# Performance work log

Measured on AMD Instinct MI355X. Metric: run time of the kernel, lower is better.

The kernel has to match this reference:

```python
import jax, jax.numpy as jnp
import numpy as np

N_RES = 320
C_Z = 128
NUM_HEAD = 4
HEAD_DIM = C_Z // NUM_HEAD  # 32
LN_EPS = 1e-5


def layer_norm(x, scale, offset):
    mean = jnp.mean(x, axis=-1, keepdims=True)
    var = jnp.var(x, axis=-1, keepdims=True)
    return (x - mean) * jax.lax.rsqrt(var + LN_EPS) * scale + offset


def setup_inputs() -> dict:
    key = jax.random.key(0)
    ks = jax.random.split(key, 12)
    d = {
        'pair_act': jax.random.normal(ks[0], (N_RES, N_RES, C_Z), jnp.float32),
        'affine_act': jax.random.normal(ks[1], (N_RES, N_RES, C_Z), jnp.float32),
        'pair_mask': jnp.ones((N_RES, N_RES), jnp.float32),
        'pair_ln_scale': jnp.ones((C_Z,), jnp.float32),
        'pair_ln_offset': jnp.zeros((C_Z,), jnp.float32),
        'affine_ln_scale': jnp.ones((C_Z,), jnp.float32),
        'affine_ln_offset': jnp.zeros((C_Z,), jnp.float32),
        'feat_2d_weights': jax.random.normal(ks[2], (C_Z, NUM_HEAD), jnp.float32) / 0.8796256610342398,
        'query_w': jax.random.normal(ks[3], (C_Z, NUM_HEAD, HEAD_DIM), jnp.float32) * 0.05,
        'key_w': jax.random.normal(ks[4], (C_Z, NUM_HEAD, HEAD_DIM), jnp.float32) * 0.05,
        'value_w': jax.random.normal(ks[5], (C_Z, NUM_HEAD, HEAD_DIM), jnp.float32) * 0.05,
        'gating_w': jax.random.normal(ks[6], (C_Z, NUM_HEAD, HEAD_DIM), jnp.float32) * 0.05,
        'output_w': jax.random.normal(ks[7], (NUM_HEAD, HEAD_DIM, C_Z), jnp.float32) * 0.05,
    }
    return d


def reference(pair_act, affine_act, pair_mask,
              pair_ln_scale, pair_ln_offset, affine_ln_scale, affine_ln_offset,
              feat_2d_weights, query_w, key_w, value_w, gating_w, output_w):
    # orientation == 'per_row' -> no swapaxes
    pair_ln = layer_norm(pair_act, pair_ln_scale, pair_ln_offset)          # [N,N,c]
    affine_ln = layer_norm(affine_act, affine_ln_scale, affine_ln_offset)  # [N,N,c]

    # padding bias [N,1,1,N]
    bias = (1e9 * (pair_mask - 1.0))[:, None, None, :]
    # nonbatched pair bias [H,N,N]
    nonbatched_bias = jnp.einsum('qkc,ch->hqk', affine_ln, feat_2d_weights)

    # attention (q_data == m_data == pair_ln)
    scale = HEAD_DIM ** (-0.5)
    q = jnp.einsum('bqa,ahc->bqhc', pair_ln, query_w) * scale
    k = jnp.einsum('bka,ahc->bkhc', pair_ln, key_w)
    v = jnp.einsum('bka,ahc->bkhc', pair_ln, value_w)

    logits = jnp.einsum('bqhc,bkhc->bhqk', q, k) + bias + nonbatched_bias[None]
    weights = jax.nn.softmax(logits, axis=-1)
    weighted_avg = jnp.einsum('bhqk,bkhc->bqhc', weights, v)

    gate = jax.nn.sigmoid(jnp.einsum('bqc,chv->bqhv', pair_ln, gating_w))
    weighted_avg = weighted_avg * gate

    out = jnp.einsum('bqhc,hco->bqo', weighted_avg, output_w)  # [N,N,c_z]
    return out
```

## Files before the change

### kernel.cpp

```cpp
#include <hip/hip_runtime.h>
#include <hip/hip_bf16.h>

#define N_RES 320
#define C_Z   128
#define NH    4
#define HD    32
#define M_TOT (N_RES*N_RES)
#define LN_EPS 1e-5f
#define QSCALE 0.17677669529663687f

typedef __attribute__((ext_vector_type(8))) short short8;
typedef __attribute__((ext_vector_type(4))) float floatx4;

#define OFF_MASK 0
#define OFF_PLS  102400
#define OFF_PLO  102528
#define OFF_ALS  102656
#define OFF_ALO  102784
#define OFF_FWT  102912
#define OFF_WQT  104960
#define OFF_WKT  121344
#define OFF_WVT  137728
#define OFF_WGT  154112
#define OFF_WOT  170496
#define ARENA_N  186880

__device__ __forceinline__ float u16_to_f(unsigned short s){
    union { unsigned u; float f; } v; v.u = ((unsigned)s) << 16; return v.f;
}
__device__ __forceinline__ unsigned short bf16r(float f){
    union { __hip_bfloat16 b; unsigned short s; } v; v.b = __float2bfloat16(f); return v.s;
}
__device__ __forceinline__ unsigned pack2(float a, float b){
    return (unsigned)bf16r(a) | ((unsigned)bf16r(b) << 16);
}
__device__ __forceinline__ float ld_dual(const void* s, size_t i, bool isbf){
    return isbf ? u16_to_f(((const unsigned short*)s)[i]) : ((const float*)s)[i];
}

__global__ __launch_bounds__(256) void k_conv_all(
    const void* __restrict__ s_mask, const void* __restrict__ s_pls,
    const void* __restrict__ s_plo,  const void* __restrict__ s_als,
    const void* __restrict__ s_alo,  const void* __restrict__ s_fw,
    const void* __restrict__ s_wq,   const void* __restrict__ s_wk,
    const void* __restrict__ s_wv,   const void* __restrict__ s_wg,
    const void* __restrict__ s_wo,
    unsigned short* __restrict__ arena, const unsigned* __restrict__ probe)
{
    int gid = blockIdx.x * 256 + threadIdx.x;
    bool isbf = (probe[0] & 0xffffu) != 0;
    float val;
    if (gid < OFF_PLS)      val = ld_dual(s_mask, gid, isbf);
    else if (gid < OFF_PLO) val = ld_dual(s_pls, gid - OFF_PLS, isbf);
    else if (gid < OFF_ALS) val = ld_dual(s_plo, gid - OFF_PLO, isbf);
    else if (gid < OFF_ALO) val = ld_dual(s_als, gid - OFF_ALS, isbf);
    else if (gid < OFF_FWT) val = ld_dual(s_alo, gid - OFF_ALO, isbf);
    else if (gid < OFF_WQT){
        int local = gid - OFF_FWT, hh = local >> 7, c = local & 127;
        val = (hh < 4) ? ld_dual(s_fw, c*NH + hh, isbf) : 0.0f;
    } else if (gid < OFF_WOT){
        int seg = (gid - OFF_WQT) >> 14;
        int local = (gid - OFF_WQT) & 16383;
        int hc = local >> 7, z = local & 127;
        const void* src = (seg == 0) ? s_wq : (seg == 1) ? s_wk : (seg == 2) ? s_wv : s_wg;
        val = ld_dual(src, z*128 + hc, isbf);
    } else {
        int local = gid - OFF_WOT, o = local >> 7, hc = local & 127;
        val = ld_dual(s_wo, hc*128 + o, isbf);
    }
    arena[gid] = bf16r(val);
}

__global__ __launch_bounds__(256) void k_affine_ln_nb(
    const void* __restrict__ affine,
    const unsigned short* __restrict__ sc, const unsigned short* __restrict__ of,
    const unsigned short* __restrict__ fwpT, float* __restrict__ nb,
    const unsigned* __restrict__ probe)
{
    int tid = threadIdx.x, lane = tid & 63, wave = tid >> 6;
    int c16 = lane & 15, quad = lane >> 4, rb = quad * 4;
    int m0 = blockIdx.x * 64 + wave * 16;
    bool isbf = (probe[0] & 0xffffu) != 0;

    float x[32];
    if (isbf){
        const short8* a8 = (const short8*)affine;
        #pragma unroll
        for (int ks = 0; ks < 4; ++ks){
            short8 t = a8[(size_t)(m0 + c16)*16 + ks*4 + quad];
            #pragma unroll
            for (int j = 0; j < 8; ++j) x[ks*8+j] = u16_to_f((unsigned short)t[j]);
        }
    } else {
        const floatx4* a4 = (const floatx4*)affine;
        #pragma unroll
        for (int ks = 0; ks < 4; ++ks){
            floatx4 f0 = a4[(size_t)(m0 + c16)*32 + ks*8 + quad*2];
            floatx4 f1 = a4[(size_t)(m0 + c16)*32 + ks*8 + quad*2 + 1];
            #pragma unroll
            for (int j = 0; j < 4; ++j){ x[ks*8+j] = f0[j]; x[ks*8+4+j] = f1[j]; }
        }
    }
    float s = 0.f, ss = 0.f;
    #pragma unroll
    for (int j = 0; j < 32; ++j){ s += x[j]; ss += x[j]*x[j]; }
    s  += __shfl_xor(s, 16, 64);  s  += __shfl_xor(s, 32, 64);
    ss += __shfl_xor(ss, 16, 64); ss += __shfl_xor(ss, 32, 64);
    float mean = s * (1.0f/128.0f);
    float var  = ss * (1.0f/128.0f) - mean*mean;
    float rs   = rsqrtf(var + LN_EPS);

    const short8* sc8 = (const short8*)sc;
    const short8* of8 = (const short8*)of;
    short8 lf[4], lg[4];
    #pragma unroll
    for (int ks = 0; ks < 4; ++ks){
        short8 scv = sc8[ks*4 + quad], ofv = of8[ks*4 + quad];
        #pragma unroll
        for (int j = 0; j < 8; ++j){
            float l = (x[ks*8+j] - mean) * rs * u16_to_f((unsigned short)scv[j])
                    + u16_to_f((unsigned short)ofv[j]);
            unsigned short hi = bf16r(l);
            lf[ks][j] = (short)hi;
            lg[ks][j] = (short)bf16r(l - u16_to_f(hi));
        }
    }
    floatx4 acc = {0.f, 0.f, 0.f, 0.f};
    const short8* fw8 = (const short8*)fwpT;
    #pragma unroll
    for (int ks = 0; ks < 4; ++ks){
        short8 fwf = fw8[c16*16 + ks*4 + quad];
        acc = __builtin_amdgcn_mfma_f32_16x16x32_bf16(lf[ks], fwf, acc, 0, 0, 0);
        acc = __builtin_amdgcn_mfma_f32_16x16x32_bf16(lg[ks], fwf, acc, 0, 0, 0);
    }
    if (c16 < 4)
        *(floatx4*)&nb[(size_t)c16 * M_TOT + m0 + rb] = acc;
}

__global__ __launch_bounds__(256) void k_pair_ln(
    const void* __restrict__ pair,
    const unsigned short* __restrict__ sc, const unsigned short* __restrict__ of,
    unsigned short* __restrict__ pl, const unsigned* __restrict__ probe)
{
    int tid = threadIdx.x, lane = tid & 63, wave = tid >> 6;
    int c16 = lane & 15, quad = lane >> 4;
    int m0 = blockIdx.x * 64 + wave * 16;
    bool isbf = (probe[0] & 0xffffu) != 0;

    float x[32];
    if (isbf){
        const short8* a8 = (const short8*)pair;
        #pragma unroll
        for (int ks = 0; ks < 4; ++ks){
            short8 t = a8[(size_t)(m0 + c16)*16 + ks*4 + quad];
            #pragma unroll
            for (int j = 0; j < 8; ++j) x[ks*8+j] = u16_to_f((unsigned short)t[j]);
        }
    } else {
        const floatx4* a4 = (const floatx4*)pair;
        #pragma unroll
        for (int ks = 0; ks < 4; ++ks){
            floatx4 f0 = a4[(size_t)(m0 + c16)*32 + ks*8 + quad*2];
            floatx4 f1 = a4[(size_t)(m0 + c16)*32 + ks*8 + quad*2 + 1];
            #pragma unroll
            for (int j = 0; j < 4; ++j){ x[ks*8+j] = f0[j]; x[ks*8+4+j] = f1[j]; }
        }
    }
    float s = 0.f, ss = 0.f;
    #pragma unroll
    for (int j = 0; j < 32; ++j){ s += x[j]; ss += x[j]*x[j]; }
    s  += __shfl_xor(s, 16, 64);  s  += __shfl_xor(s, 32, 64);
    ss += __shfl_xor(ss, 16, 64); ss += __shfl_xor(ss, 32, 64);
    float mean = s * (1.0f/128.0f);
    float var  = ss * (1.0f/128.0f) - mean*mean;
    float rs   = rsqrtf(var + LN_EPS);

    const short8* sc8 = (const short8*)sc;
    const short8* of8 = (const short8*)of;
    short8* pl8 = (short8*)pl;
    #pragma unroll
    for (int ks = 0; ks < 4; ++ks){
        short8 scv = sc8[ks*4 + quad], ofv = of8[ks*4 + quad];
        short8 lf;
        #pragma unroll
        for (int j = 0; j < 8; ++j){
            float l = (x[ks*8+j] - mean) * rs * u16_to_f((unsigned short)scv[j])
                    + u16_to_f((unsigned short)ofv[j]);
            lf[j] = (short)bf16r(l);
        }
        pl8[(size_t)(m0 + c16)*16 + ks*4 + quad] = lf;
    }
}

__global__ __launch_bounds__(512, 4) void k_attn(
    const unsigned short* __restrict__ pl,
    const unsigned short* __restrict__ wqT, const unsigned short* __restrict__ wkT,
    const unsigned short* __restrict__ wvT, const unsigned short* __restrict__ wgT,
    const unsigned short* __restrict__ maskc, const float* __restrict__ nb,
    unsigned short* __restrict__ wab)
{
    __shared__ __align__(16) unsigned short Ks[320*40];
    __shared__ __align__(16) unsigned short Vt[32*328];
    __shared__ __align__(16) unsigned short Pbuf[8*640];
    __shared__ __align__(16) float biasl[320];

    int b = blockIdx.x, h = blockIdx.y;
    int tid = threadIdx.x, lane = tid & 63, wave = tid >> 6;
    int c16 = lane & 15, quad = lane >> 4, rb = quad * 4;

    const short8* plrow8 = (const short8*)(pl + (size_t)b * N_RES * C_Z);
    const short8* Ks8 = (const short8*)Ks;
    const short8* Vt8 = (const short8*)Vt;
    const short8* wqT8 = (const short8*)wqT;
    const short8* wgT8 = (const short8*)wgT;
    unsigned short* Pw = Pbuf + wave * 640;
    const short8* Pb8 = (const short8*)Pw;
    floatx4 Z = {0.f, 0.f, 0.f, 0.f};

    if (tid < 320)
        biasl[tid] = 1e9f * (u16_to_f(maskc[(size_t)b * N_RES + tid]) - 1.0f);

    #pragma unroll 1
    for (int t = wave; t < 80; t += 8){
        int isV = (t >= 40) ? 1 : 0;
        int r = isV ? t - 40 : t;
        int ct = (r >= 20) ? 1 : 0;
        int mt = (r >= 20) ? r - 20 : r;
        int hc = h*HD + ct*16 + c16;
        const short8* WT8 = (const short8*)(isV ? wvT : wkT);
        short8 bw[4], a[4];
        #pragma unroll
        for (int ks = 0; ks < 4; ++ks){
            bw[ks] = WT8[hc*16 + ks*4 + quad];
            a[ks]  = plrow8[(mt*16 + c16)*16 + ks*4 + quad];
        }
        floatx4 acc = Z;
        if (!isV){
            #pragma unroll
            for (int ks = 0; ks < 4; ++ks)
                acc = __builtin_amdgcn_mfma_f32_16x16x32_bf16(a[ks], bw[ks], acc, 0, 0, 0);
            #pragma unroll
            for (int i = 0; i < 4; ++i)
                Ks[(mt*16 + rb + i)*40 + ct*16 + c16] = bf16r(acc[i]);
        } else {
            #pragma unroll
            for (int ks = 0; ks < 4; ++ks)
                acc = __builtin_amdgcn_mfma_f32_16x16x32_bf16(bw[ks], a[ks], acc, 0, 0, 0);
            #pragma unroll
            for (int i = 0; i < 4; ++i)
                Vt[(ct*16 + rb + i)*328 + mt*16 + c16] = bf16r(acc[i]);
        }
    }
    __syncthreads();

    #pragma unroll 1
    for (int mt = wave; mt < 20; mt += 8){
        int m0 = mt * 16;
        short8 plf[4];
        #pragma unroll
        for (int ks = 0; ks < 4; ++ks)
            plf[ks] = plrow8[(m0 + c16)*16 + ks*4 + quad];

        floatx4 q0 = Z, q1 = Z;
        #pragma unroll
        for (int ks = 0; ks < 4; ++ks){
            short8 w0 = wqT8[(h*HD + c16)*16 + ks*4 + quad];
            short8 w1 = wqT8[(h*HD + 16 + c16)*16 + ks*4 + quad];
            q0 = __builtin_amdgcn_mfma_f32_16x16x32_bf16(w0, plf[ks], q0, 0, 0, 0);
            q1 = __builtin_amdgcn_mfma_f32_16x16x32_bf16(w1, plf[ks], q1, 0, 0, 0);
        }
        {
            uint2 pk0 = { pack2(q0[0]*QSCALE, q0[1]*QSCALE), pack2(q0[2]*QSCALE, q0[3]*QSCALE) };
            uint2 pk1 = { pack2(q1[0]*QSCALE, q1[1]*QSCALE), pack2(q1[2]*QSCALE, q1[3]*QSCALE) };
            *(uint2*)&Pw[c16*40 + quad*4]      = pk0;
            *(uint2*)&Pw[c16*40 + 16 + quad*4] = pk1;
        }
        short8 qf = Pb8[c16*5 + quad];

        float mrow = -3.0e38f, lrow = 0.f;
        floatx4 acc0 = Z, acc1 = Z;
        const float* nbq = nb + (size_t)h * M_TOT + (size_t)(m0 + c16) * N_RES;

        #pragma unroll 1
        for (int kt2 = 0; kt2 < 10; ++kt2){
            int k0 = kt2 * 32;
            short8 kfa = Ks8[(k0 + c16)*5 + quad];
            short8 kfb = Ks8[(k0 + 16 + c16)*5 + quad];
            floatx4 sa = __builtin_amdgcn_mfma_f32_16x16x32_bf16(kfa, qf, Z, 0, 0, 0);
            floatx4 sb = __builtin_amdgcn_mfma_f32_16x16x32_bf16(kfb, qf, Z, 0, 0, 0);
            floatx4 nba = *(const floatx4*)&nbq[k0 + quad*4];
            floatx4 nbb = *(const floatx4*)&nbq[k0 + 16 + quad*4];
            floatx4 bia = *(const floatx4*)&biasl[k0 + quad*4];
            floatx4 bib = *(const floatx4*)&biasl[k0 + 16 + quad*4];
            float tm = -3.0e38f;
            #pragma unroll
            for (int i = 0; i < 4; ++i){
                sa[i] += nba[i] + bia[i];
                sb[i] += nbb[i] + bib[i];
                tm = fmaxf(tm, fmaxf(sa[i], sb[i]));
            }
            tm = fmaxf(tm, __shfl_xor(tm, 16, 64));
            tm = fmaxf(tm, __shfl_xor(tm, 32, 64));
            float mn = fmaxf(mrow, tm);
            float alpha = __expf(mrow - mn);
            mrow = mn;
            float pa[4], pb[4], tsum = 0.f;
            #pragma unroll
            for (int i = 0; i < 4; ++i){
                pa[i] = __expf(sa[i] - mn);
                pb[i] = __expf(sb[i] - mn);
                tsum += pa[i] + pb[i];
            }
            tsum += __shfl_xor(tsum, 16, 64);
            tsum += __shfl_xor(tsum, 32, 64);
            lrow = lrow * alpha + tsum;
            uint2 wa = { pack2(pa[0], pa[1]), pack2(pa[2], pa[3]) };
            uint2 wb = { pack2(pb[0], pb[1]), pack2(pb[2], pb[3]) };
            *(uint2*)&Pw[c16*40 + quad*4]      = wa;
            *(uint2*)&Pw[c16*40 + 16 + quad*4] = wb;
            short8 pf = Pb8[c16*5 + quad];
            short8 v0 = Vt8[c16*41 + kt2*4 + quad];
            short8 v1 = Vt8[(16 + c16)*41 + kt2*4 + quad];
            #pragma unroll
            for (int i = 0; i < 4; ++i){
                float al = __shfl(alpha, rb + i, 64);
                acc0[i] *= al; acc1[i] *= al;
            }
            acc0 = __builtin_amdgcn_mfma_f32_16x16x32_bf16(pf, v0, acc0, 0, 0, 0);
            acc1 = __builtin_amdgcn_mfma_f32_16x16x32_bf16(pf, v1, acc1, 0, 0, 0);
        }

        floatx4 g0 = Z, g1 = Z;
        #pragma unroll
        for (int ks = 0; ks < 4; ++ks){
            short8 w0 = wgT8[(h*HD + c16)*16 + ks*4 + quad];
            short8 w1 = wgT8[(h*HD + 16 + c16)*16 + ks*4 + quad];
            g0 = __builtin_amdgcn_mfma_f32_16x16x32_bf16(plf[ks], w0, g0, 0, 0, 0);
            g1 = __builtin_amdgcn_mfma_f32_16x16x32_bf16(plf[ks], w1, g1, 0, 0, 0);
        }
        #pragma unroll
        for (int i = 0; i < 4; ++i){
            float li = __shfl(lrow, rb + i, 64);
            float inv = 1.0f / li;
            float o0 = acc0[i] * inv * (1.0f/(1.0f + __expf(-g0[i])));
            float o1 = acc1[i] * inv * (1.0f/(1.0f + __expf(-g1[i])));
            size_t orow = (size_t)h * (M_TOT*HD) + (size_t)(b*N_RES + m0 + rb + i) * HD;
            wab[orow + c16]      = bf16r(o0);
            wab[orow + 16 + c16] = bf16r(o1);
        }
    }
}

__global__ __launch_bounds__(256, 4) void k_outproj(
    const unsigned short* __restrict__ wab, const unsigned short* __restrict__ woT,
    void* __restrict__ out, const unsigned* __restrict__ probe)
{
    int tid = threadIdx.x, lane = tid & 63, wave = tid >> 6;
    int c16 = lane & 15, quad = lane >> 4, rb = quad * 4;
    int m0 = blockIdx.x * 64 + wave * 16;
    bool isbf = (probe[0] & 0xffffu) != 0;

    const short8* wab8 = (const short8*)wab;
    const short8* woT8 = (const short8*)woT;
    floatx4 Z = {0.f, 0.f, 0.f, 0.f};

    short8 a[4];
    #pragma unroll
    for (int ks = 0; ks < 4; ++ks)
        a[ks] = wab8[(size_t)ks * (M_TOT*4) + (size_t)(m0 + c16)*4 + quad];

    #pragma unroll 1
    for (int nt = 0; nt < 8; ++nt){
        floatx4 acc = Z;
        #pragma unroll
        for (int ks = 0; ks < 4; ++ks){
            short8 bf = woT8[(nt*16 + c16)*16 + ks*4 + quad];
            acc = __builtin_amdgcn_mfma_f32_16x16x32_bf16(a[ks], bf, acc, 0, 0, 0);
        }
        #pragma unroll
        for (int i = 0; i < 4; ++i){
            size_t idx = (size_t)(m0 + rb + i)*C_Z + nt*16 + c16;
            if (isbf) ((unsigned short*)out)[idx] = bf16r(acc[i]);
            else      ((float*)out)[idx] = acc[i];
        }
    }
}

extern "C" void kernel_launch(void* const* d_in, const int* in_sizes, int n_in,
                              void* d_out, int out_size, void* d_ws, size_t ws_size,
                              hipStream_t stream)
{
    const unsigned* probe = (const unsigned*)d_in[3];

    char* w = (char*)d_ws;
    unsigned short* arena = (unsigned short*)w;
    unsigned short* mask_c = arena + OFF_MASK;
    unsigned short* pls_c  = arena + OFF_PLS;
    unsigned short* plo_c  = arena + OFF_PLO;
    unsigned short* als_c  = arena + OFF_ALS;
    unsigned short* alo_c  = arena + OFF_ALO;
    unsigned short* fwT_c  = arena + OFF_FWT;
    unsigned short* wqT_c  = arena + OFF_WQT;
    unsigned short* wkT_c  = arena + OFF_WKT;
    unsigned short* wvT_c  = arena + OFF_WVT;
    unsigned short* wgT_c  = arena + OFF_WGT;
    unsigned short* woT_c  = arena + OFF_WOT;
    float*          nb     = (float*)(w + 524288);
    unsigned short* pl     = (unsigned short*)(w + 2162688);
    unsigned short* wab    = (unsigned short*)(w + 28377088);

    k_conv_all<<<730, 256, 0, stream>>>(d_in[2], d_in[3], d_in[4], d_in[5], d_in[6],
                                        d_in[7], d_in[8], d_in[9], d_in[10], d_in[11],
                                        d_in[12], arena, probe);
    k_affine_ln_nb<<<1600, 256, 0, stream>>>(d_in[1], als_c, alo_c, fwT_c, nb, probe);
    k_pair_ln    <<<1600, 256, 0, stream>>>(d_in[0], pls_c, plo_c, pl, probe);
    k_attn       <<<dim3(N_RES, NH), 512, 0, stream>>>(pl, wqT_c, wkT_c, wvT_c, wgT_c,
                                                       mask_c, nb, wab);
    k_outproj    <<<1600, 256, 0, stream>>>(wab, woT_c, d_out, probe);
}
```

Before: 416.8 us.

## Replace LDS P/Q staging with cross-lane permlane transposes, fold log2e into exp2

Result: slower. 444.2 us (+6.6%).

```diff
diff --git a/kernel.cpp b/kernel.cpp
--- a/kernel.cpp
+++ b/kernel.cpp
@@ -8,9 +8,11 @@
 #define M_TOT (N_RES*N_RES)
 #define LN_EPS 1e-5f
 #define QSCALE 0.17677669529663687f
+#define LOG2E  1.4426950408889634f
 
 typedef __attribute__((ext_vector_type(8))) short short8;
 typedef __attribute__((ext_vector_type(4))) float floatx4;
+typedef __attribute__((ext_vector_type(4))) unsigned uintx4;
 
 #define OFF_MASK 0
 #define OFF_PLS  102400
@@ -36,6 +38,32 @@
 }
 __device__ __forceinline__ float ld_dual(const void* s, size_t i, bool isbf){
     return isbf ? u16_to_f(((const unsigned short*)s)[i]) : ((const float*)s)[i];
+}
+
+__device__ __forceinline__ short8 xpose_frag(unsigned A0, unsigned A1,
+                                             unsigned B0, unsigned B1, int lane)
+{
+#if __has_builtin(__builtin_amdgcn_permlane32_swap) && __has_builtin(__builtin_amdgcn_permlane16_swap)
+    (void)lane;
+    auto uv0 = __builtin_amdgcn_permlane32_swap(A0, B0, false, false);
+    auto uv1 = __builtin_amdgcn_permlane32_swap(A1, B1, false, false);
+    auto t02 = __builtin_amdgcn_permlane16_swap(uv0[0], uv0[1], false, false);
+    auto t13 = __builtin_amdgcn_permlane16_swap(uv1[0], uv1[1], false, false);
+    uintx4 u = { t02[0], t13[0], t02[1], t13[1] };
+#else
+    bool hi32 = lane >= 32, oddq = (lane & 16) != 0;
+    unsigned A0x = __shfl_xor(A0, 32, 64), B0x = __shfl_xor(B0, 32, 64);
+    unsigned A1x = __shfl_xor(A1, 32, 64), B1x = __shfl_xor(B1, 32, 64);
+    unsigned U0 = hi32 ? B0x : A0, V0 = hi32 ? B0 : A0x;
+    unsigned U1 = hi32 ? B1x : A1, V1 = hi32 ? B1 : A1x;
+    unsigned U0x = __shfl_xor(U0, 16, 64), V0x = __shfl_xor(V0, 16, 64);
+    unsigned U1x = __shfl_xor(U1, 16, 64), V1x = __shfl_xor(V1, 16, 64);
+    unsigned T0 = oddq ? V0x : U0, T2 = oddq ? V0 : U0x;
+    unsigned T1 = oddq ? V1x : U1, T3 = oddq ? V1 : U1x;
+    uintx4 u = { T0, T1, T2, T3 };
+#endif
+    union { uintx4 u; short8 s; } cvt; cvt.u = u;
+    return cvt.s;
 }
 
 __global__ __launch_bounds__(256) void k_conv_all(
@@ -133,6 +161,7 @@
         acc = __builtin_amdgcn_mfma_f32_16x16x32_bf16(lf[ks], fwf, acc, 0, 0, 0);
         acc = __builtin_amdgcn_mfma_f32_16x16x32_bf16(lg[ks], fwf, acc, 0, 0, 0);
     }
+    acc = acc * LOG2E;
     if (c16 < 4)
         *(floatx4*)&nb[(size_t)c16 * M_TOT + m0 + rb] = acc;
 }
@@ -192,7 +221,7 @@
     }
 }
 
-__global__ __launch_bounds__(512, 4) void k_attn(
+__global__ __launch_bounds__(512, 6) void k_attn(
     const unsigned short* __restrict__ pl,
     const unsigned short* __restrict__ wqT, const unsigned short* __restrict__ wkT,
     const unsigned short* __restrict__ wvT, const unsigned short* __restrict__ wgT,
@@ -201,7 +230,6 @@
 {
     __shared__ __align__(16) unsigned short Ks[320*40];
     __shared__ __align__(16) unsigned short Vt[32*328];
-    __shared__ __align__(16) unsigned short Pbuf[8*640];
     __shared__ __align__(16) float biasl[320];
 
     int b = blockIdx.x, h = blockIdx.y;
@@ -213,12 +241,10 @@
     const short8* Vt8 = (const short8*)Vt;
     const short8* wqT8 = (const short8*)wqT;
     const short8* wgT8 = (const short8*)wgT;
-    unsigned short* Pw = Pbuf + wave * 640;
-    const short8* Pb8 = (const short8*)Pw;
     floatx4 Z = {0.f, 0.f, 0.f, 0.f};
 
     if (tid < 320)
-        biasl[tid] = 1e9f * (u16_to_f(maskc[(size_t)b * N_RES + tid]) - 1.0f);
+        biasl[tid] = (LOG2E * 1e9f) * (u16_to_f(maskc[(size_t)b * N_RES + tid]) - 1.0f);
 
     #pragma unroll 1
     for (int t = wave; t < 80; t += 8){
@@ -261,23 +287,23 @@
         for (int ks = 0; ks < 4; ++ks)
             plf[ks] = plrow8[(m0 + c16)*16 + ks*4 + quad];
 
-        floatx4 q0 = Z, q1 = Z;
+        floatx4 q0 = Z, q1 = Z, g0v = Z, g1v = Z;
         #pragma unroll
         for (int ks = 0; ks < 4; ++ks){
             short8 w0 = wqT8[(h*HD + c16)*16 + ks*4 + quad];
             short8 w1 = wqT8[(h*HD + 16 + c16)*16 + ks*4 + quad];
             q0 = __builtin_amdgcn_mfma_f32_16x16x32_bf16(w0, plf[ks], q0, 0, 0, 0);
             q1 = __builtin_amdgcn_mfma_f32_16x16x32_bf16(w1, plf[ks], q1, 0, 0, 0);
-        }
-        {
-            uint2 pk0 = { pack2(q0[0]*QSCALE, q0[1]*QSCALE), pack2(q0[2]*QSCALE, q0[3]*QSCALE) };
-            uint2 pk1 = { pack2(q1[0]*QSCALE, q1[1]*QSCALE), pack2(q1[2]*QSCALE, q1[3]*QSCALE) };
-            *(uint2*)&Pw[c16*40 + quad*4]      = pk0;
-            *(uint2*)&Pw[c16*40 + 16 + quad*4] = pk1;
-        }
-        short8 qf = Pb8[c16*5 + quad];
-
-        float mrow = -3.0e38f, lrow = 0.f;
+            short8 u0 = wgT8[(h*HD + c16)*16 + ks*4 + quad];
+            short8 u1 = wgT8[(h*HD + 16 + c16)*16 + ks*4 + quad];
+            g0v = __builtin_amdgcn_mfma_f32_16x16x32_bf16(u0, plf[ks], g0v, 0, 0, 0);
+            g1v = __builtin_amdgcn_mfma_f32_16x16x32_bf16(u1, plf[ks], g1v, 0, 0, 0);
+        }
+        const float QS = QSCALE * LOG2E;
+        short8 qf = xpose_frag(pack2(q0[0]*QS, q0[1]*QS), pack2(q0[2]*QS, q0[3]*QS),
+                               pack2(q1[0]*QS, q1[1]*QS), pack2(q1[2]*QS, q1[3]*QS), lane);
+
+        float mrow = -3.0e38f, lpart = 0.f;
         floatx4 acc0 = Z, acc1 = Z;
         const float* nbq = nb + (size_t)h * M_TOT + (size_t)(m0 + c16) * N_RES;
 
@@ -288,66 +314,54 @@
             short8 kfb = Ks8[(k0 + 16 + c16)*5 + quad];
             floatx4 sa = __builtin_amdgcn_mfma_f32_16x16x32_bf16(kfa, qf, Z, 0, 0, 0);
             floatx4 sb = __builtin_amdgcn_mfma_f32_16x16x32_bf16(kfb, qf, Z, 0, 0, 0);
-            floatx4 nba = *(const floatx4*)&nbq[k0 + quad*4];
-            floatx4 nbb = *(const floatx4*)&nbq[k0 + 16 + quad*4];
-            floatx4 bia = *(const floatx4*)&biasl[k0 + quad*4];
-            floatx4 bib = *(const floatx4*)&biasl[k0 + 16 + quad*4];
-            float tm = -3.0e38f;
+            floatx4 nba = *(const floatx4*)&nbq[k0 + rb];
+            floatx4 nbb = *(const floatx4*)&nbq[k0 + 16 + rb];
+            floatx4 bia = *(const floatx4*)&biasl[k0 + rb];
+            floatx4 bib = *(const floatx4*)&biasl[k0 + 16 + rb];
             #pragma unroll
             for (int i = 0; i < 4; ++i){
                 sa[i] += nba[i] + bia[i];
                 sb[i] += nbb[i] + bib[i];
-                tm = fmaxf(tm, fmaxf(sa[i], sb[i]));
             }
+            float tm = fmaxf(fmaxf(fmaxf(sa[0], sa[1]), fmaxf(sa[2], sa[3])),
+                             fmaxf(fmaxf(sb[0], sb[1]), fmaxf(sb[2], sb[3])));
             tm = fmaxf(tm, __shfl_xor(tm, 16, 64));
             tm = fmaxf(tm, __shfl_xor(tm, 32, 64));
             float mn = fmaxf(mrow, tm);
-            float alpha = __expf(mrow - mn);
+            float alpha = exp2f(mrow - mn);
             mrow = mn;
-            float pa[4], pb[4], tsum = 0.f;
+            float pa[4], pb[4], ts = 0.f;
             #pragma unroll
             for (int i = 0; i < 4; ++i){
-                pa[i] = __expf(sa[i] - mn);
-                pb[i] = __expf(sb[i] - mn);
-                tsum += pa[i] + pb[i];
+                pa[i] = exp2f(sa[i] - mn);
+                pb[i] = exp2f(sb[i] - mn);
+                ts += pa[i] + pb[i];
             }
-            tsum += __shfl_xor(tsum, 16, 64);
-            tsum += __shfl_xor(tsum, 32, 64);
-            lrow = lrow * alpha + tsum;
-            uint2 wa = { pack2(pa[0], pa[1]), pack2(pa[2], pa[3]) };
-            uint2 wb = { pack2(pb[0], pb[1]), pack2(pb[2], pb[3]) };
-            *(uint2*)&Pw[c16*40 + quad*4]      = wa;
-            *(uint2*)&Pw[c16*40 + 16 + quad*4] = wb;
-            short8 pf = Pb8[c16*5 + quad];
+            lpart = lpart * alpha + ts;
+            short8 pt = xpose_frag(pack2(pa[0], pa[1]), pack2(pa[2], pa[3]),
+                                   pack2(pb[0], pb[1]), pack2(pb[2], pb[3]), lane);
             short8 v0 = Vt8[c16*41 + kt2*4 + quad];
             short8 v1 = Vt8[(16 + c16)*41 + kt2*4 + quad];
             #pragma unroll
-            for (int i = 0; i < 4; ++i){
-                float al = __shfl(alpha, rb + i, 64);
-                acc0[i] *= al; acc1[i] *= al;
-            }
-            acc0 = __builtin_amdgcn_mfma_f32_16x16x32_bf16(pf, v0, acc0, 0, 0, 0);
-            acc1 = __builtin_amdgcn_mfma_f32_16x16x32_bf16(pf, v1, acc1, 0, 0, 0);
-        }
-
-        floatx4 g0 = Z, g1 = Z;
-        #pragma unroll
-        for (int ks = 0; ks < 4; ++ks){
-            short8 w0 = wgT8[(h*HD + c16)*16 + ks*4 + quad];
-            short8 w1 = wgT8[(h*HD + 16 + c16)*16 + ks*4 + quad];
-            g0 = __builtin_amdgcn_mfma_f32_16x16x32_bf16(plf[ks], w0, g0, 0, 0, 0);
-            g1 = __builtin_amdgcn_mfma_f32_16x16x32_bf16(plf[ks], w1, g1, 0, 0, 0);
-        }
+            for (int i = 0; i < 4; ++i){ acc0[i] *= alpha; acc1[i] *= alpha; }
+            acc0 = __builtin_amdgcn_mfma_f32_16x16x32_bf16(v0, pt, acc0, 0, 0, 0);
+            acc1 = __builtin_amdgcn_mfma_f32_16x16x32_bf16(v1, pt, acc1, 0, 0, 0);
+        }
+
+        lpart += __shfl_xor(lpart, 16, 64);
+        lpart += __shfl_xor(lpart, 32, 64);
+        float inv = 1.0f / lpart;
+        float o[8];
         #pragma unroll
         for (int i = 0; i < 4; ++i){
-            float li = __shfl(lrow, rb + i, 64);
-            float inv = 1.0f / li;
-            float o0 = acc0[i] * inv * (1.0f/(1.0f + __expf(-g0[i])));
-            float o1 = acc1[i] * inv * (1.0f/(1.0f + __expf(-g1[i])));
-            size_t orow = (size_t)h * (M_TOT*HD) + (size_t)(b*N_RES + m0 + rb + i) * HD;
-            wab[orow + c16]      = bf16r(o0);
-            wab[orow + 16 + c16] = bf16r(o1);
-        }
+            o[i]     = acc0[i] * inv * (1.0f/(1.0f + __expf(-g0v[i])));
+            o[4 + i] = acc1[i] * inv * (1.0f/(1.0f + __expf(-g1v[i])));
+        }
+        size_t base = (size_t)h * (M_TOT*HD) + (size_t)(b*N_RES + m0 + c16) * HD;
+        uint2 s0 = { pack2(o[0], o[1]), pack2(o[2], o[3]) };
+        uint2 s1 = { pack2(o[4], o[5]), pack2(o[6], o[7]) };
+        *(uint2*)&wab[base + rb]      = s0;
+        *(uint2*)&wab[base + 16 + rb] = s1;
     }
 }
 
```
